# Performance work log

Measured on AMD Instinct MI355X. Metric: run time of the kernel, lower is better.

The kernel has to match this reference:

```python
import jax, jax.numpy as jnp
import numpy as np

N_NODES = 50000
N_REL = 256
D_IN = 128
NHID = 128
NHEADS = 2
D_OUT = NHID * NHEADS  # 256
ALPHA = 0.2  # leakyrelu slope


def _l2norm(x, eps=1e-12):
    n = jnp.sqrt(jnp.sum(x * x, axis=1, keepdims=True))
    return x / jnp.maximum(n, eps)


def _gat_layer(x, edge, edge_embed, a, a2, num_nodes, concat):
    """KBGAT-style sparse attention layer.
    x: [N, d_in]; edge: [2, E] (row0=dst, row1=src); edge_embed: [E, d_rel]
    a: [d_out, 2*d_in + d_rel]; a2: [d_out].
    Returns (h, h_raw, rowsum) ~ (x, x_l, x_w) of the original layer.
    """
    d_in = x.shape[1]
    dst, src = edge[0], edge[1]
    # edge_m = a @ cat(x[dst], x[src], edge_embed).T, computed blockwise -> [E, d_out]
    a_d, a_s, a_r = a[:, :d_in], a[:, d_in:2 * d_in], a[:, 2 * d_in:]
    edge_m = x[dst] @ a_d.T + x[src] @ a_s.T + edge_embed @ a_r.T
    # attention logits: exp(-leakyrelu(a2 . edge_m))
    powers = -jax.nn.leaky_relu(edge_m @ a2, negative_slope=ALPHA)  # [E]
    edge_e = jnp.exp(powers)
    rowsum = jax.ops.segment_sum(edge_e, dst, num_segments=num_nodes)  # [N]
    rowsum = jnp.where(rowsum == 0, 1e-12, rowsum)
    h_raw = jax.ops.segment_sum(edge_e[:, None] * edge_m, dst, num_segments=num_nodes)  # [N, d_out]
    h = h_raw / rowsum[:, None]
    if concat:
        h = jax.nn.elu(h)
    return h, h_raw, rowsum[:, None]


def setup_inputs() -> dict:
    key = jax.random.key(0)
    ks = jax.random.split(key, 16)
    E, E_NHOP = 300000, 30000
    xav = lambda k, shp: jax.random.uniform(k, shp, jnp.float32, -1.0, 1.0) * (
        1.414 * np.sqrt(6.0 / (shp[-2] + shp[-1])))
    inp = {
        "entity_embeddings": jax.random.normal(ks[0], (N_NODES, D_IN), jnp.float32),
        "relation_embeddings": jax.random.normal(ks[1], (N_REL, D_IN), jnp.float32),
        # per-head layer-1 attention params (stacked over heads)
        "a1": xav(ks[2], (NHEADS, NHID, 2 * D_IN + D_IN)),
        "a2_1": xav(ks[3], (NHEADS, NHID)),
        "W": xav(ks[4], (D_IN, D_OUT)),          # relation projection in SpGAT
        "a_out": xav(ks[5], (D_OUT, 2 * D_OUT + D_OUT)),
        "a2_out": xav(ks[6], (1, D_OUT))[0],
        "W_entities": xav(ks[7], (D_IN, D_OUT)),
        "batch_inputs": jax.random.randint(ks[8], (4096, 3), 0, N_NODES),
        "edge_list": jax.random.randint(ks[9], (2, E), 0, N_NODES),
        "edge_type": jax.random.randint(ks[10], (E,), 0, N_REL),
        "edge_list_nhop": jax.random.randint(ks[11], (2, E_NHOP), 0, N_NODES),
        "edge_type_nhop": jax.random.randint(ks[12], (E_NHOP, 2), 0, N_REL),
    }
    return inp


def reference(entity_embeddings, relation_embeddings, a1, a2_1, W, a_out, a2_out,
              W_entities, batch_inputs, edge_list, edge_type, edge_list_nhop,
              edge_type_nhop):
    # in-place row normalization of entity embeddings (as in original forward)
    ent = _l2norm(entity_embeddings)
    edge_all = jnp.concatenate([edge_list, edge_list_nhop], axis=1)  # [2, E+Enh]

    # ---- SpGAT layer 1: multi-head over original relation embeddings ----
    edge_embed = relation_embeddings[edge_type]
    edge_embed_nhop = relation_embeddings[edge_type_nhop[:, 0]] + relation_embeddings[edge_type_nhop[:, 1]]
    ee_all = jnp.concatenate([edge_embed, edge_embed_nhop], axis=0)
    heads = [
        _gat_layer(ent, edge_all, ee_all, a1[h], a2_1[h], N_NODES, concat=True)[0]
        for h in range(NHEADS)
    ]
    x = jnp.concatenate(heads, axis=1)  # [N, NHEADS*NHID]

    # ---- relation projection + output attention layer ----
    out_relation_1 = relation_embeddings @ W  # [R, D_OUT]
    ee2 = out_relation_1[edge_type]
    ee2_nhop = out_relation_1[edge_type_nhop[:, 0]] + out_relation_1[edge_type_nhop[:, 1]]
    ee2_all = jnp.concatenate([ee2, ee2_nhop], axis=0)
    xo, x_l, x_w = _gat_layer(x, edge_all, ee2_all, a_out, a2_out, N_NODES, concat=False)
    xo, x_l, x_w = jax.nn.elu(xo), jax.nn.elu(x_l), jax.nn.elu(x_w)

    # ---- residual mask update + normalization ----
    mask = jnp.zeros((N_NODES,), xo.dtype).at[batch_inputs[:, 2]].set(1.0)
    entities_upgraded = ent @ W_entities
    out_entity_1 = entities_upgraded + mask[:, None] * xo
    out_entity_1 = _l2norm(out_entity_1)
    out_entity_l_1 = _l2norm(x_l)
    return (out_entity_1, out_relation_1, out_entity_l_1)
```

## Files before the change

kernel.cpp:

```cpp
#include <hip/hip_runtime.h>
#include <hip/hip_bf16.h>
#include <math.h>

#define N_NODES 50000
#define E1 300000
#define EN 30000
#define ETOT 330000

typedef __hip_bfloat16 bf16;

__device__ __forceinline__ float b2f(bf16 x){ return __bfloat162float(x); }
__device__ __forceinline__ bf16 f2b(float x){ return __float2bfloat16(x); }

__device__ __forceinline__ float ldf(const void* p, long i, bool f32){
  return f32 ? ((const float*)p)[i] : b2f(((const bf16*)p)[i]);
}
__device__ __forceinline__ void stf(void* p, long i, float v, bool f32){
  if (f32) ((float*)p)[i] = v; else ((bf16*)p)[i] = f2b(v);
}
__device__ __forceinline__ void stv4(void* p, long elem, float a, float b,
                                     float c, float d, bool f32){
  if (f32){
    float4 t; t.x=a; t.y=b; t.z=c; t.w=d;
    *reinterpret_cast<float4*>((float*)p + elem) = t;
  } else {
    bf16 t[4] = {f2b(a), f2b(b), f2b(c), f2b(d)};
    *reinterpret_cast<uint2*>((bf16*)p + elem) = *reinterpret_cast<uint2*>(t);
  }
}

__global__ void k_detect(const void* __restrict__ emb, int* __restrict__ flag){
  const unsigned short* h = (const unsigned short*)emb;
  int sane = 0;
  for (int i=0;i<128;i++){
    unsigned e = (h[i]>>7)&0xFFu;
    if (e>=112u && e<=143u) sane++;
  }
  *flag = (sane >= 112) ? 0 : 1;
}

__global__ void k_hist(const int* __restrict__ el, const int* __restrict__ eln,
                       int* __restrict__ cnt){
  int i = blockIdx.x*blockDim.x + threadIdx.x;
  if (i < ETOT){
    int dst = (i < E1) ? el[i] : eln[i - E1];
    atomicAdd(cnt + dst, 1);
  }
}

__global__ __launch_bounds__(1024) void k_scan(const int* __restrict__ cnt,
                                               int* __restrict__ rowp,
                                               int* __restrict__ cur){
  __shared__ int part[1024];
  int t = threadIdx.x;
  const int CH = (N_NODES + 1023)/1024;
  int base = t*CH;
  int s = 0;
  for (int i=0;i<CH;i++){ int n = base+i; if (n < N_NODES) s += cnt[n]; }
  part[t] = s;
  __syncthreads();
  for (int o=1;o<1024;o<<=1){
    int u = (t>=o) ? part[t-o] : 0;
    __syncthreads();
    part[t] += u;
    __syncthreads();
  }
  int off = part[t] - s;
  for (int i=0;i<CH;i++){
    int n = base+i;
    if (n < N_NODES){ rowp[n] = off; cur[n] = off; off += cnt[n]; }
  }
  if (t==0) rowp[N_NODES] = ETOT;
}

__global__ void k_fill(const int* __restrict__ el, const int* __restrict__ et,
                       const int* __restrict__ eln, const int* __restrict__ etn,
                       int* __restrict__ cur, int* __restrict__ esrc,
                       int* __restrict__ epak){
  int i = blockIdx.x*blockDim.x + threadIdx.x;
  if (i >= ETOT) return;
  int dst, src, pk;
  if (i < E1){
    dst = el[i]; src = el[E1 + i];
    pk = et[i];
  } else {
    int e = i - E1;
    dst = eln[e]; src = eln[EN + e];
    pk = etn[2*e] | (etn[2*e+1]<<9) | (1<<18);
  }
  int pos = atomicAdd(cur + dst, 1);
  esrc[pos] = src; epak[pos] = pk;
}

__global__ __launch_bounds__(256) void k_gath1(
    const int* __restrict__ rowp, const int* __restrict__ esrc,
    const int* __restrict__ epak,
    const float* __restrict__ pd, const float* __restrict__ ps,
    const float* __restrict__ rp,
    const float* __restrict__ sd, const float* __restrict__ ss,
    const float* __restrict__ sr,
    float* __restrict__ x, int hoff){
  int w = threadIdx.x >> 6, lane = threadIdx.x & 63;
  int n = blockIdx.x*4 + w;
  if (n >= N_NODES) return;
  const float2* ps2 = (const float2*)ps;
  const float2* rp2 = (const float2*)rp;
  float2 acc; acc.x = 0.f; acc.y = 0.f;
  float rs = 0.f;
  float sdn = sd[n];
  int b = rowp[n], e = rowp[n+1];
  for (int i=b;i<e;i++){
    int src = esrc[i], pk = epak[i];
    int t0 = pk & 511, t1 = (pk>>9)&511, has2 = (pk>>18)&1;
    float srv = sr[t0] + (has2 ? sr[t1] : 0.f);
    float score = sdn + ss[src] + srv;
    float lr = score > 0.f ? score : 0.2f*score;
    float wgt = expf(-lr);
    rs += wgt;
    float2 v  = ps2[(long)src*64 + lane];
    float2 r1 = rp2[(long)t0*64 + lane];
    v.x += r1.x; v.y += r1.y;
    if (has2){ float2 r2v = rp2[(long)t1*64 + lane]; v.x += r2v.x; v.y += r2v.y; }
    acc.x += wgt*v.x; acc.y += wgt*v.y;
  }
  float denom = (rs == 0.f) ? 1e-12f : rs;
  float2 pdv = ((const float2*)pd)[(long)n*64 + lane];
  float hr0 = rs*pdv.x + acc.x, hr1 = rs*pdv.y + acc.y;
  float h0 = hr0/denom; h0 = h0 > 0.f ? h0 : (expf(h0) - 1.f);
  float h1 = hr1/denom; h1 = h1 > 0.f ? h1 : (expf(h1) - 1.f);
  float2 o; o.x = h0; o.y = h1;
  *reinterpret_cast<float2*>(x + (long)n*256 + hoff + lane*2) = o;
}

__global__ __launch_bounds__(256) void k_gath2(
    const int* __restrict__ rowp, const int* __restrict__ esrc,
    const int* __restrict__ epak,
    const float* __restrict__ p2d, const float* __restrict__ ps,
    const float* __restrict__ rp,
    const float* __restrict__ sd, const float* __restrict__ ss,
    const float* __restrict__ sr,
    const float* __restrict__ eu, const float* __restrict__ mask,
    const int* __restrict__ flag, void* __restrict__ out){
  bool f32 = flag[0] != 0;
  int w = threadIdx.x >> 6, lane = threadIdx.x & 63;
  int n = blockIdx.x*4 + w;
  if (n >= N_NODES) return;
  const float4* ps4 = (const float4*)ps;
  const float4* rp4 = (const float4*)rp;
  float4 acc; acc.x=acc.y=acc.z=acc.w=0.f;
  float rs = 0.f;
  float sdn = sd[n];
  int b = rowp[n], e = rowp[n+1];
  for (int i=b;i<e;i++){
    int src = esrc[i], pk = epak[i];
    int t0 = pk & 511, t1 = (pk>>9)&511, has2 = (pk>>18)&1;
    float srv = sr[t0] + (has2 ? sr[t1] : 0.f);
    float score = sdn + ss[src] + srv;
    float lr = score > 0.f ? score : 0.2f*score;
    float wgt = expf(-lr);
    rs += wgt;
    float4 v  = ps4[(long)src*64 + lane];
    float4 r1 = rp4[(long)t0*64 + lane];
    v.x += r1.x; v.y += r1.y; v.z += r1.z; v.w += r1.w;
    if (has2){
      float4 r2v = rp4[(long)t1*64 + lane];
      v.x += r2v.x; v.y += r2v.y; v.z += r2v.z; v.w += r2v.w;
    }
    acc.x += wgt*v.x; acc.y += wgt*v.y; acc.z += wgt*v.z; acc.w += wgt*v.w;
  }
  float denom = (rs == 0.f) ? 1e-12f : rs;
  float mk = mask[n];
  float4 pdv = ((const float4*)p2d)[(long)n*64 + lane];
  float4 euv = ((const float4*)eu)[(long)n*64 + lane];
  float av[4] = {acc.x, acc.y, acc.z, acc.w};
  float pv[4] = {pdv.x, pdv.y, pdv.z, pdv.w};
  float ev[4] = {euv.x, euv.y, euv.z, euv.w};
  float val[4], xl[4];
  float n1 = 0.f, n2 = 0.f;
  #pragma unroll
  for (int m=0;m<4;m++){
    float hr = rs*pv[m] + av[m];
    float xo = hr/denom; xo = xo > 0.f ? xo : (expf(xo) - 1.f);
    float l  = hr > 0.f ? hr : (expf(hr) - 1.f);
    float v  = ev[m] + mk*xo;
    val[m] = v; xl[m] = l;
    n1 += v*v; n2 += l*l;
  }
  #pragma unroll
  for (int o=32;o>0;o>>=1){ n1 += __shfl_xor(n1,o); n2 += __shfl_xor(n2,o); }
  float i1 = 1.f/fmaxf(sqrtf(n1), 1e-12f);
  float i2 = 1.f/fmaxf(sqrtf(n2), 1e-12f);
  stv4(out, (long)n*256 + lane*4,
       val[0]*i1, val[1]*i1, val[2]*i1, val[3]*i1, f32);
  stv4(out, 12865536L + (long)n*256 + lane*4,
       xl[0]*i2, xl[1]*i2, xl[2]*i2, xl[3]*i2, f32);
}

__global__ void k_rel2(const void* __restrict__ rel, const void* __restrict__ W,
                       const int* __restrict__ flag,
                       float* __restrict__ r2, void* __restrict__ out){
  bool f32 = flag[0] != 0;
  int t = blockIdx.x, j = threadIdx.x;
  __shared__ float rs_[128];
  if (j < 128) rs_[j] = ldf(rel, (long)t*128 + j, f32);
  __syncthreads();
  float acc = 0.f;
  #pragma unroll 4
  for (int k=0;k<128;k++) acc += rs_[k]*ldf(W, (long)k*256 + j, f32);
  r2[(long)t*256+j] = acc;
  stf(out, 12800000L + (long)t*256 + j, acc, f32);
}

__global__ void k_trF(const void* __restrict__ src, const int* __restrict__ flag,
                      long bias, long jstride, int J, float* __restrict__ dst){
  bool f32 = flag[0] != 0;
  int k = blockIdx.x, j = threadIdx.x;
  dst[(long)k*J + j] = ldf(src, bias + (long)j*jstride + k, f32);
}

__global__ void k_cvtF(const void* __restrict__ src, const int* __restrict__ flag,
                       int n, float* __restrict__ dst){
  bool f32 = flag[0] != 0;
  int i = blockIdx.x*blockDim.x + threadIdx.x;
  if (i < n) dst[i] = ldf(src, i, f32);
}

__global__ void k_comb(float* __restrict__ a, float* __restrict__ b, int n){
  int i = blockIdx.x*blockDim.x + threadIdx.x;
  if (i < n){ a[i] += a[n+i]; b[i] += b[n+i]; }
}

template<int NT, int K, int KT, int BM, int NCOL, int COLS_TOT,
         int NORM, int DUAL, int SCORE, int XDUAL>
__global__ __launch_bounds__(NT) void k_gnp(
    const void* __restrict__ X, const int* __restrict__ flag, int N,
    const float* __restrict__ WT1, const float* __restrict__ WT2,
    const void* __restrict__ a2, long a2bias,
    float* __restrict__ O1, float* __restrict__ O2,
    float* __restrict__ s1, float* __restrict__ s2){
  const int COLS  = 64*NCOL;
  const int WAVES = NT/64;
  const int RW    = BM/WAVES;
  __shared__ __align__(16) float xs[BM][KT];
  __shared__ float rsc[BM];
  int t = threadIdx.x;
  int wv = t >> 6, ln = t & 63;
  int r0 = wv * RW;
  int n0 = blockIdx.x * BM;
  int coff = blockIdx.y * COLS;
  bool xf32 = XDUAL ? (flag[0] != 0) : true;

  float a1c[RW][NCOL], a2c[RW][NCOL];
  #pragma unroll
  for (int m=0;m<RW;m++)
    #pragma unroll
    for (int c=0;c<NCOL;c++){ a1c[m][c]=0.f; a2c[m][c]=0.f; }

  for (int kt0 = 0; kt0 < K; kt0 += KT){
    if (xf32){
      const int KQ = KT/4;
      for (int idx = t; idx < BM*KQ; idx += NT){
        int m = idx / KQ, kq = idx - m*KQ;
        int n = n0 + m;
        float4 v; v.x=v.y=v.z=v.w=0.f;
        if (n < N)
          v = *reinterpret_cast<const float4*>((const float*)X + (long)n*K + kt0 + kq*4);
        *reinterpret_cast<float4*>(&xs[m][kq*4]) = v;
      }
    } else {
      for (int idx = t; idx < BM*KT; idx += NT){
        int m = idx / KT, k = idx - m*KT;
        int n = n0 + m;
        xs[m][k] = (n < N) ? b2f(((const bf16*)X)[(long)n*K + kt0 + k]) : 0.f;
      }
    }
    __syncthreads();

    if (NORM){
      const int NPR = NT / BM;
      int r = t / NPR, l = t - r*NPR;
      float ssq = 0.f;
      #pragma unroll
      for (int k = l; k < KT; k += NPR){ float v = xs[r][k]; ssq += v*v; }
      #pragma unroll
      for (int o = NPR>>1; o > 0; o >>= 1) ssq += __shfl_xor(ssq, o);
      if (l == 0) rsc[r] = 1.f / fmaxf(sqrtf(ssq), 1e-12f);
      __syncthreads();
      for (int idx = t; idx < BM*KT; idx += NT){
        int m = idx / KT, k = idx - m*KT;
        xs[m][k] *= rsc[m];
      }
      __syncthreads();
    }

    #pragma unroll 1
    for (int k0=0;k0<KT;k0+=4){
      float w1v[4][NCOL], w2v[4][NCOL];
      #pragma unroll
      for (int i=0;i<4;i++){
        const float* p1 = WT1 + (long)(kt0+k0+i)*COLS_TOT + coff + ln*NCOL;
        if constexpr (NCOL==4){
          float4 v = *reinterpret_cast<const float4*>(p1);
          w1v[i][0]=v.x; w1v[i][1]=v.y; w1v[i][2]=v.z; w1v[i][3]=v.w;
        } else {
          float2 v = *reinterpret_cast<const float2*>(p1);
          w1v[i][0]=v.x; w1v[i][1]=v.y;
        }
        if (DUAL){
          const float* p2 = WT2 + (long)(kt0+k0+i)*COLS_TOT + coff + ln*NCOL;
          if constexpr (NCOL==4){
            float4 v = *reinterpret_cast<const float4*>(p2);
            w2v[i][0]=v.x; w2v[i][1]=v.y; w2v[i][2]=v.z; w2v[i][3]=v.w;
          } else {
            float2 v = *reinterpret_cast<const float2*>(p2);
            w2v[i][0]=v.x; w2v[i][1]=v.y;
          }
        }
      }
      #pragma unroll
      for (int m=0;m<RW;m++){
        float4 xv = *reinterpret_cast<const float4*>(&xs[r0+m][k0]);
        #pragma unroll
        for (int c=0;c<NCOL;c++){
          a1c[m][c] += xv.x*w1v[0][c] + xv.y*w1v[1][c] + xv.z*w1v[2][c] + xv.w*w1v[3][c];
          if (DUAL)
            a2c[m][c] += xv.x*w2v[0][c] + xv.y*w2v[1][c] + xv.z*w2v[2][c] + xv.w*w2v[3][c];
        }
      }
    }
    __syncthreads();
  }

  #pragma unroll
  for (int m=0;m<RW;m++){
    int n = n0 + r0 + m;
    if (n < N){
      float* o1 = O1 + (long)n*COLS_TOT + coff + ln*NCOL;
      if constexpr (NCOL==4){
        float4 v; v.x=a1c[m][0]; v.y=a1c[m][1]; v.z=a1c[m][2]; v.w=a1c[m][3];
        *reinterpret_cast<float4*>(o1) = v;
      } else {
        float2 v; v.x=a1c[m][0]; v.y=a1c[m][1];
        *reinterpret_cast<float2*>(o1) = v;
      }
      if (DUAL){
        float* o2 = O2 + (long)n*COLS_TOT + coff + ln*NCOL;
        if constexpr (NCOL==4){
          float4 v; v.x=a2c[m][0]; v.y=a2c[m][1]; v.z=a2c[m][2]; v.w=a2c[m][3];
          *reinterpret_cast<float4*>(o2) = v;
        } else {
          float2 v; v.x=a2c[m][0]; v.y=a2c[m][1];
          *reinterpret_cast<float2*>(o2) = v;
        }
      }
    }
  }

  if (SCORE){
    bool af32 = flag[0] != 0;
    float a2v[NCOL];
    #pragma unroll
    for (int c=0;c<NCOL;c++) a2v[c] = ldf(a2, a2bias + coff + ln*NCOL + c, af32);
    long soff = (long)blockIdx.y * N;
    #pragma unroll
    for (int m=0;m<RW;m++){
      float v1 = 0.f, v2 = 0.f;
      #pragma unroll
      for (int c=0;c<NCOL;c++){
        v1 += a1c[m][c]*a2v[c];
        if (DUAL) v2 += a2c[m][c]*a2v[c];
      }
      #pragma unroll
      for (int o=32;o>0;o>>=1){
        v1 += __shfl_down(v1,o);
        if (DUAL) v2 += __shfl_down(v2,o);
      }
      int n = n0 + r0 + m;
      if (ln==0 && n < N){
        s1[soff + n] = v1;
        if (DUAL) s2[soff + n] = v2;
      }
    }
  }
}

__global__ void k_mask(const int* __restrict__ bi, float* __restrict__ mask){
  int i = blockIdx.x*blockDim.x + threadIdx.x;
  if (i < 4096) mask[bi[i*3 + 2]] = 1.f;
}

extern "C" void kernel_launch(void* const* d_in, const int* in_sizes, int n_in,
                              void* d_out, int out_size, void* d_ws, size_t ws_size,
                              hipStream_t stream) {
  const void* emb = d_in[0];
  const void* rel = d_in[1];
  const void* a1b = d_in[2];
  const void* a21 = d_in[3];
  const void* W   = d_in[4];
  const void* aout= d_in[5];
  const void* a2o = d_in[6];
  const void* We  = d_in[7];
  const int* bi   = (const int*)d_in[8];
  const int* el   = (const int*)d_in[9];
  const int* et   = (const int*)d_in[10];
  const int* eln  = (const int*)d_in[11];
  const int* etn  = (const int*)d_in[12];
  float* ws = (float*)d_ws;

  const size_t PD_=0, PS_=6400000;
  const size_t P2D_=0;
  const size_t CNT_=12800000, ROWP_=12860000, ESRC_=12920000, EPAK_=13260000;
  const size_t TW_=19200000;
  const size_t X_=25600000;
  const size_t P2S_=38400000;
  const size_t SD_=51250000, SS_=51300000, S2D_=51350000,
               S2S_=51400000, MK_=51500000,
               RP1_=51550000, SR1_=51590000, R2_=51600000, RP2_=51670000,
               SR2_=51740000, FLAG_=51750000;
  int* flag = (int*)(ws + FLAG_);
  int* cnt  = (int*)(ws + CNT_);
  int* rowp = (int*)(ws + ROWP_);
  int* esrc = (int*)(ws + ESRC_);
  int* epak = (int*)(ws + EPAK_);

  k_detect<<<1,1,0,stream>>>(emb, flag);

  hipMemsetAsync(ws+MK_,  0, (size_t)50000*sizeof(float), stream);
  hipMemsetAsync(cnt,     0, (size_t)50000*sizeof(int), stream);

  k_hist<<<(ETOT+255)/256,256,0,stream>>>(el, eln, cnt);
  k_scan<<<1,1024,0,stream>>>(cnt, rowp, cnt);
  k_fill<<<(ETOT+255)/256,256,0,stream>>>(el, et, eln, etn, cnt, esrc, epak);

  k_trF<<<128,128,0,stream>>>(a1b, flag, 0L,          384L, 128, ws+TW_);
  k_trF<<<128,128,0,stream>>>(a1b, flag, 128L,        384L, 128, ws+TW_+16384);
  k_trF<<<128,128,0,stream>>>(a1b, flag, 49152L,      384L, 128, ws+TW_+32768);
  k_trF<<<128,128,0,stream>>>(a1b, flag, 49152L+128L, 384L, 128, ws+TW_+49152);
  k_trF<<<128,128,0,stream>>>(a1b, flag, 256L,        384L, 128, ws+TW_+65536);
  k_trF<<<128,128,0,stream>>>(a1b, flag, 49152L+256L, 384L, 128, ws+TW_+81920);

  k_gnp<256,128,128,32,2,128,1,1,1,1><<<dim3((N_NODES+31)/32,1),256,0,stream>>>(
      emb, flag, N_NODES, ws+TW_, ws+TW_+16384, a21, 0L,
      ws+PD_, ws+PS_, ws+SD_, ws+SS_);
  k_gnp<256,128,128,64,2,128,0,0,1,1><<<dim3(4,1),256,0,stream>>>(
      rel, flag, 256, ws+TW_+65536, nullptr, a21, 0L,
      ws+RP1_, nullptr, ws+SR1_, nullptr);
  k_gath1<<<(N_NODES+3)/4,256,0,stream>>>(rowp, esrc, epak,
      ws+PD_, ws+PS_, ws+RP1_, ws+SD_, ws+SS_, ws+SR1_, ws+X_, 0);

  k_gnp<256,128,128,32,2,128,1,1,1,1><<<dim3((N_NODES+31)/32,1),256,0,stream>>>(
      emb, flag, N_NODES, ws+TW_+32768, ws+TW_+49152, a21, 128L,
      ws+PD_, ws+PS_, ws+SD_, ws+SS_);
  k_gnp<256,128,128,64,2,128,0,0,1,1><<<dim3(4,1),256,0,stream>>>(
      rel, flag, 256, ws+TW_+81920, nullptr, a21, 128L,
      ws+RP1_, nullptr, ws+SR1_, nullptr);
  k_gath1<<<(N_NODES+3)/4,256,0,stream>>>(rowp, esrc, epak,
      ws+PD_, ws+PS_, ws+RP1_, ws+SD_, ws+SS_, ws+SR1_, ws+X_, 128);

  k_rel2<<<256,256,0,stream>>>(rel, W, flag, ws+R2_, d_out);

  k_trF<<<256,256,0,stream>>>(aout, flag, 0L,   768L, 256, ws+TW_);
  k_trF<<<256,256,0,stream>>>(aout, flag, 256L, 768L, 256, ws+TW_+65536);
  k_trF<<<256,256,0,stream>>>(aout, flag, 512L, 768L, 256, ws+TW_+131072);

  k_gnp<256,256,128,64,4,256,0,0,1,0><<<dim3(4,1),256,0,stream>>>(
      ws+R2_, flag, 256, ws+TW_+131072, nullptr, a2o, 0L,
      ws+RP2_, nullptr, ws+SR2_, nullptr);

  k_gnp<256,256,128,64,2,256,0,1,1,0><<<dim3((N_NODES+63)/64,2),256,0,stream>>>(
      ws+X_, flag, N_NODES, ws+TW_, ws+TW_+65536, a2o, 0L,
      ws+P2D_, ws+P2S_, ws+SD_, ws+S2D_);
  k_comb<<<(N_NODES+255)/256,256,0,stream>>>(ws+SD_, ws+S2D_, N_NODES);

  k_cvtF<<<128,256,0,stream>>>(We, flag, 32768, ws+RP1_);
  k_mask<<<16,256,0,stream>>>(bi, ws+MK_);
  k_gnp<256,128,128,32,4,256,1,0,0,1><<<dim3((N_NODES+31)/32,1),256,0,stream>>>(
      emb, flag, N_NODES, ws+RP1_, nullptr, nullptr, 0L,
      ws+X_, nullptr, nullptr, nullptr);

  k_gath2<<<(N_NODES+3)/4,256,0,stream>>>(rowp, esrc, epak,
      ws+P2D_, ws+P2S_, ws+RP2_, ws+SD_, ws+S2D_, ws+SR2_,
      ws+X_, ws+MK_, flag, d_out);
}
```

Before: 1.100 ms.

## Compute output-layer node projections with split-bf16 MFMA instead of scalar FP32

```diff
diff --git a/kernel.cpp b/kernel.cpp
--- a/kernel.cpp
+++ b/kernel.cpp
@@ -8,9 +8,15 @@
 #define ETOT 330000
 
 typedef __hip_bfloat16 bf16;
+typedef __attribute__((ext_vector_type(8))) short s8v;
+typedef __attribute__((ext_vector_type(4))) float f4v;
 
 __device__ __forceinline__ float b2f(bf16 x){ return __bfloat162float(x); }
 __device__ __forceinline__ bf16 f2b(float x){ return __float2bfloat16(x); }
+
+__device__ __forceinline__ f4v mfma16(s8v a, s8v b, f4v c){
+  return __builtin_amdgcn_mfma_f32_16x16x32_bf16(a, b, c, 0, 0, 0);
+}
 
 __device__ __forceinline__ float ldf(const void* p, long i, bool f32){
   return f32 ? ((const float*)p)[i] : b2f(((const bf16*)p)[i]);
@@ -218,6 +224,17 @@
   dst[(long)k*J + j] = ldf(src, bias + (long)j*jstride + k, f32);
 }
 
+__global__ void k_wfrag(const void* __restrict__ src, const int* __restrict__ flag,
+                        long bias, long jstride, int K,
+                        bf16* __restrict__ whi, bf16* __restrict__ wlo){
+  bool f32 = flag[0] != 0;
+  int c = blockIdx.x, k = threadIdx.x;
+  float w = ldf(src, bias + (long)c*jstride + k, f32);
+  bf16 h = f2b(w);
+  whi[(long)c*K + k] = h;
+  wlo[(long)c*K + k] = f2b(w - b2f(h));
+}
+
 __global__ void k_cvtF(const void* __restrict__ src, const int* __restrict__ flag,
                        int n, float* __restrict__ dst){
   bool f32 = flag[0] != 0;
@@ -225,9 +242,103 @@
   if (i < n) dst[i] = ldf(src, i, f32);
 }
 
-__global__ void k_comb(float* __restrict__ a, float* __restrict__ b, int n){
-  int i = blockIdx.x*blockDim.x + threadIdx.x;
-  if (i < n){ a[i] += a[n+i]; b[i] += b[n+i]; }
+__global__ __launch_bounds__(256) void k_gm2(
+    const float* __restrict__ X, int N,
+    const bf16* __restrict__ whd, const bf16* __restrict__ wld,
+    const bf16* __restrict__ whs, const bf16* __restrict__ wls,
+    const void* __restrict__ a2, const int* __restrict__ flag,
+    float* __restrict__ O1, float* __restrict__ O2,
+    float* __restrict__ s1, float* __restrict__ s2){
+  __shared__ __align__(16) bf16 xhi[64*256];
+  __shared__ __align__(16) bf16 xlo[64*256];
+  int t = threadIdx.x, wv = t>>6, ln = t&63;
+  int n0 = blockIdx.x*64;
+
+  for (int i = t; i < 64*64; i += 256){
+    int row = i >> 6, kq = i & 63;
+    int n = n0 + row;
+    float4 v; v.x=v.y=v.z=v.w=0.f;
+    if (n < N) v = *reinterpret_cast<const float4*>(X + (long)n*256 + kq*4);
+    bf16 h[4], l[4];
+    h[0]=f2b(v.x); l[0]=f2b(v.x-b2f(h[0]));
+    h[1]=f2b(v.y); l[1]=f2b(v.y-b2f(h[1]));
+    h[2]=f2b(v.z); l[2]=f2b(v.z-b2f(h[2]));
+    h[3]=f2b(v.w); l[3]=f2b(v.w-b2f(h[3]));
+    long byo = ((long)row*512 + kq*8) ^ ((row&7)<<4);
+    *reinterpret_cast<uint2*>(reinterpret_cast<char*>(xhi)+byo) =
+        *reinterpret_cast<const uint2*>(h);
+    *reinterpret_cast<uint2*>(reinterpret_cast<char*>(xlo)+byo) =
+        *reinterpret_cast<const uint2*>(l);
+  }
+  __syncthreads();
+
+  int cl = ln & 15, rg = ln >> 4;
+  long arow = (long)(wv*16 + cl);
+  long abase = arow*512 + rg*16;
+  long aswz = (arow&7)<<4;
+  const char* xh = reinterpret_cast<const char*>(xhi);
+  const char* xl = reinterpret_cast<const char*>(xlo);
+
+  f4v accd[16], accs[16];
+  const f4v zf = {0.f,0.f,0.f,0.f};
+  #pragma unroll
+  for (int ct=0; ct<16; ++ct){ accd[ct]=zf; accs[ct]=zf; }
+
+  #pragma unroll 1
+  for (int kb=0; kb<8; ++kb){
+    s8v ah = *reinterpret_cast<const s8v*>(xh + ((abase + kb*64) ^ aswz));
+    s8v al = *reinterpret_cast<const s8v*>(xl + ((abase + kb*64) ^ aswz));
+    long kO = kb*32 + rg*8;
+    #pragma unroll
+    for (int ct=0; ct<16; ++ct){
+      long wo = (long)(ct*16 + cl)*256 + kO;
+      s8v bh = *reinterpret_cast<const s8v*>((const void*)(whd + wo));
+      s8v bl = *reinterpret_cast<const s8v*>((const void*)(wld + wo));
+      accd[ct] = mfma16(ah, bh, accd[ct]);
+      accd[ct] = mfma16(ah, bl, accd[ct]);
+      accd[ct] = mfma16(al, bh, accd[ct]);
+      s8v ch  = *reinterpret_cast<const s8v*>((const void*)(whs + wo));
+      s8v cl2 = *reinterpret_cast<const s8v*>((const void*)(wls + wo));
+      accs[ct] = mfma16(ah, ch,  accs[ct]);
+      accs[ct] = mfma16(ah, cl2, accs[ct]);
+      accs[ct] = mfma16(al, ch,  accs[ct]);
+    }
+  }
+
+  bool af32 = flag[0] != 0;
+  float sc1[4]={0.f,0.f,0.f,0.f}, sc2[4]={0.f,0.f,0.f,0.f};
+  #pragma unroll
+  for (int ct=0; ct<16; ++ct){
+    float a2v = ldf(a2, ct*16 + cl, af32);
+    #pragma unroll
+    for (int r=0;r<4;r++){ sc1[r] += accd[ct][r]*a2v; sc2[r] += accs[ct][r]*a2v; }
+  }
+  #pragma unroll
+  for (int r=0;r<4;r++){
+    int n = n0 + wv*16 + rg*4 + r;
+    if (n < N){
+      #pragma unroll
+      for (int ct=0; ct<16; ++ct){
+        O1[(long)n*256 + ct*16 + cl] = accd[ct][r];
+        O2[(long)n*256 + ct*16 + cl] = accs[ct][r];
+      }
+    }
+  }
+  #pragma unroll
+  for (int o=1;o<16;o<<=1){
+    #pragma unroll
+    for (int r=0;r<4;r++){
+      sc1[r] += __shfl_xor(sc1[r], o);
+      sc2[r] += __shfl_xor(sc2[r], o);
+    }
+  }
+  if (cl == 0){
+    #pragma unroll
+    for (int r=0;r<4;r++){
+      int n = n0 + wv*16 + rg*4 + r;
+      if (n < N){ s1[n] = sc1[r]; s2[n] = sc2[r]; }
+    }
+  }
 }
 
 template<int NT, int K, int KT, int BM, int NCOL, int COLS_TOT,
@@ -459,18 +570,18 @@
 
   k_rel2<<<256,256,0,stream>>>(rel, W, flag, ws+R2_, d_out);
 
-  k_trF<<<256,256,0,stream>>>(aout, flag, 0L,   768L, 256, ws+TW_);
-  k_trF<<<256,256,0,stream>>>(aout, flag, 256L, 768L, 256, ws+TW_+65536);
+  bf16* wb = (bf16*)(ws + TW_);
+  k_wfrag<<<256,256,0,stream>>>(aout, flag, 0L,   768L, 256, wb,        wb+65536);
+  k_wfrag<<<256,256,0,stream>>>(aout, flag, 256L, 768L, 256, wb+131072, wb+196608);
   k_trF<<<256,256,0,stream>>>(aout, flag, 512L, 768L, 256, ws+TW_+131072);
 
   k_gnp<256,256,128,64,4,256,0,0,1,0><<<dim3(4,1),256,0,stream>>>(
       ws+R2_, flag, 256, ws+TW_+131072, nullptr, a2o, 0L,
       ws+RP2_, nullptr, ws+SR2_, nullptr);
 
-  k_gnp<256,256,128,64,2,256,0,1,1,0><<<dim3((N_NODES+63)/64,2),256,0,stream>>>(
-      ws+X_, flag, N_NODES, ws+TW_, ws+TW_+65536, a2o, 0L,
-      ws+P2D_, ws+P2S_, ws+SD_, ws+S2D_);
-  k_comb<<<(N_NODES+255)/256,256,0,stream>>>(ws+SD_, ws+S2D_, N_NODES);
+  k_gm2<<<(N_NODES+63)/64,256,0,stream>>>(
+      ws+X_, N_NODES, wb, wb+65536, wb+131072, wb+196608,
+      a2o, flag, ws+P2D_, ws+P2S_, ws+S2D_, ws+S2S_);
 
   k_cvtF<<<128,256,0,stream>>>(We, flag, 32768, ws+RP1_);
   k_mask<<<16,256,0,stream>>>(bi, ws+MK_);
@@ -479,6 +590,6 @@
       ws+X_, nullptr, nullptr, nullptr);
 
   k_gath2<<<(N_NODES+3)/4,256,0,stream>>>(rowp, esrc, epak,
-      ws+P2D_, ws+P2S_, ws+RP2_, ws+SD_, ws+S2D_, ws+SR2_,
+      ws+P2D_, ws+P2S_, ws+RP2_, ws+S2D_, ws+S2S_, ws+SR2_,
       ws+X_, ws+MK_, flag, d_out);
 }
```

New measurement: 1.227 ms. +11.6%, slower.
